# Optimization experiments

Measured on AMD Instinct MI355X. Metric: run time of the kernel, lower is better.

Reference implementation:

```python
import jax, jax.numpy as jnp
import numpy as np

B, S, H2 = 32, 4096, 512  # H2 = 2*hidden_size


def setup_inputs() -> dict:
    key = jax.random.key(0)
    ks = jax.random.split(key, 10)
    s = 1.0 / np.sqrt(H2)
    return {
        "decoder_state": jax.random.normal(ks[0], (B, 1, H2), jnp.float32),
        "encoder_outputs": jax.random.normal(ks[1], (B, S, H2), jnp.float32),
        "coverage_vector": jax.random.uniform(ks[2], (B, S, H2), jnp.float32),
        "W_h": jax.random.uniform(ks[3], (H2, H2), jnp.float32, -s, s),
        "b_h": jax.random.uniform(ks[4], (H2,), jnp.float32, -s, s),
        "W_s": jax.random.uniform(ks[5], (H2, H2), jnp.float32, -s, s),
        "b_s": jax.random.uniform(ks[6], (H2,), jnp.float32, -s, s),
        "W_c": jax.random.uniform(ks[7], (H2, H2), jnp.float32, -s, s),
        "b_c": jax.random.uniform(ks[8], (H2,), jnp.float32, -s, s),
        "v": jax.random.uniform(ks[9], (H2, 1), jnp.float32, -s, s),
    }


def reference(decoder_state, encoder_outputs, coverage_vector,
              W_h, b_h, W_s, b_s, W_c, b_c, v):
    # additive attention features: [B, S, 2H]
    e = jnp.tanh(encoder_outputs @ W_h + b_h
                 + decoder_state @ W_s + b_s      # broadcasts over S
                 + coverage_vector @ W_c + b_c)
    scores = e @ v                                # [B, S, 1]
    attn_dist = jax.nn.softmax(scores, axis=1)    # softmax over source positions
    # weighted sum of encoder outputs: [B, 1, 2H]
    h_star_t = jnp.einsum('bsi,bsd->bid', attn_dist, encoder_outputs)
    coverage_new = coverage_vector + attn_dist    # broadcast over feature dim
    return h_star_t, attn_dist, coverage_new
```

## Files before the change

### kernel.cpp

```cpp
#include <hip/hip_runtime.h>
#include <hip/hip_bf16.h>
#include <stdint.h>

#define H2    512
#define BATCH 32
#define SEQ   4096
#define BM    64
#define BK    64
#define NKT   16

typedef __attribute__((ext_vector_type(4))) float f32x4;
typedef __attribute__((ext_vector_type(8))) short bf16x8;

__device__ __forceinline__ unsigned short f2bf(float f) {
    union { float f; unsigned u; } v; v.f = f;
    unsigned r = v.u + 0x7FFF + ((v.u >> 16) & 1);
    return (unsigned short)(r >> 16);
}

__device__ __forceinline__ float fast_tanh(float x) {
    float e = __builtin_amdgcn_exp2f(x * 2.88539008177793f);
    return 1.0f - 2.0f * __builtin_amdgcn_rcpf(e + 1.0f);
}

__global__ void kprep_w(const float* __restrict__ Wh, const float* __restrict__ Wc,
                        unsigned short* __restrict__ wt) {
    int c    = blockIdx.x * blockDim.x + threadIdx.x;
    int lane = c & 63;
    int cb   = (c >> 6) & 31;
    int ks   = (c >> 11) & 1;
    int kt   = c >> 12;
    int col  = cb * 16 + (lane & 15);
    int k0   = kt * 64 + ks * 32 + (lane >> 4) * 8;
    unsigned short tmp[8];
#pragma unroll
    for (int j = 0; j < 8; ++j) {
        int kg = k0 + j;
        float w = (kg < 512) ? Wh[kg * 512 + col] : Wc[(kg - 512) * 512 + col];
        tmp[j] = f2bf(w);
    }
    *reinterpret_cast<uint4*>(wt + (size_t)c * 8) = *reinterpret_cast<const uint4*>(tmp);
}

__global__ void kprep_q(const float* __restrict__ dec, const float* __restrict__ Ws,
                        const float* __restrict__ bh, const float* __restrict__ bs,
                        const float* __restrict__ bc, float* __restrict__ q) {
    __shared__ float dsh[512];
    int b = blockIdx.x, t = threadIdx.x;
    dsh[t]       = dec[b * 512 + t];
    dsh[t + 256] = dec[b * 512 + 256 + t];
    __syncthreads();
    float a0 = 0.f, a1 = 0.f;
#pragma unroll 4
    for (int k = 0; k < 512; ++k) {
        float d = dsh[k];
        a0 = fmaf(d, Ws[k * 512 + t], a0);
        a1 = fmaf(d, Ws[k * 512 + 256 + t], a1);
    }
    q[b * 512 + t]       = a0 + bh[t] + bs[t] + bc[t];
    q[b * 512 + 256 + t] = a1 + bh[256 + t] + bs[256 + t] + bc[256 + t];
}

__launch_bounds__(512, 4)
__global__ void kgemm(const float* __restrict__ enc, const float* __restrict__ cov,
                      const unsigned short* __restrict__ wt,
                      const float* __restrict__ q, const float* __restrict__ vvec,
                      float* __restrict__ scores) {
    __shared__ unsigned short Asm[2][BM * BK];
    __shared__ float qv[H2];
    __shared__ float vv[H2];
    __shared__ float sred[BM][8];

    int tid  = threadIdx.x;
    int lane = tid & 63, wn = tid >> 6;

    int cpx  = gridDim.x >> 3;
    int swz  = (blockIdx.x & 7) * cpx + (blockIdx.x >> 3);
    int row0 = swz * BM;

    qv[tid] = q[(row0 >> 12) * H2 + tid];
    vv[tid] = vvec[tid];

    int r = tid >> 3, k8 = tid & 7;
    const float* ae = enc + (size_t)(row0 + r) * H2 + k8 * 8;
    const float* ac = cov + (size_t)(row0 + r) * H2 + k8 * 8;
    unsigned awb = (unsigned)(r * 128 + ((k8 * 16) ^ ((r & 7) << 4)));

    unsigned arb0 = (unsigned)((lane & 15) * 128 +
                    ((((lane >> 4) << 4))      ^ ((lane & 7) << 4)));
    unsigned arb1 = (unsigned)((lane & 15) * 128 +
                    (((64 + ((lane >> 4) << 4))) ^ ((lane & 7) << 4)));

    f32x4 acc[4][4] = {};

    {
        f32x4 a0 = *reinterpret_cast<const f32x4*>(ae);
        f32x4 a1 = *reinterpret_cast<const f32x4*>(ae + 4);
        union { unsigned short h[8]; uint4 u; } t;
#pragma unroll
        for (int j = 0; j < 4; ++j) { t.h[j] = f2bf(a0[j]); t.h[4 + j] = f2bf(a1[j]); }
        *reinterpret_cast<uint4*>((char*)Asm[0] + awb) = t.u;
    }
    __syncthreads();

    for (int kt = 0; kt < NKT; ++kt) {
        int cur = kt & 1;
        bf16x8 bfr[2][4];
        const bf16x8* bp0 = reinterpret_cast<const bf16x8*>(wt) +
                            ((size_t)(kt * 2 + 0) * 32 + wn * 4) * 64 + lane;
        const bf16x8* bp1 = reinterpret_cast<const bf16x8*>(wt) +
                            ((size_t)(kt * 2 + 1) * 32 + wn * 4) * 64 + lane;
#pragma unroll
        for (int ni = 0; ni < 4; ++ni) bfr[0][ni] = bp0[ni * 64];
#pragma unroll
        for (int ni = 0; ni < 4; ++ni) bfr[1][ni] = bp1[ni * 64];
        f32x4 p0, p1;
        if (kt + 1 < NKT) {
            const float* src = (kt + 1 < 8) ? (ae + (kt + 1) * 64) : (ac + (kt - 7) * 64);
            p0 = *reinterpret_cast<const f32x4*>(src);
            p1 = *reinterpret_cast<const f32x4*>(src + 4);
        }
#pragma unroll
        for (int ks = 0; ks < 2; ++ks) {
            bf16x8 af[4];
#pragma unroll
            for (int mi = 0; mi < 4; ++mi)
                af[mi] = *reinterpret_cast<const bf16x8*>(
                    (const char*)Asm[cur] + mi * 2048 + (ks ? arb1 : arb0));
#pragma unroll
            for (int mi = 0; mi < 4; ++mi)
#pragma unroll
                for (int ni = 0; ni < 4; ++ni)
                    acc[mi][ni] = __builtin_amdgcn_mfma_f32_16x16x32_bf16(
                        af[mi], bfr[ks][ni], acc[mi][ni], 0, 0, 0);
        }
        if (kt + 1 < NKT) {
            union { unsigned short h[8]; uint4 u; } t;
#pragma unroll
            for (int j = 0; j < 4; ++j) { t.h[j] = f2bf(p0[j]); t.h[4 + j] = f2bf(p1[j]); }
            *reinterpret_cast<uint4*>((char*)Asm[cur ^ 1] + awb) = t.u;
        }
        __syncthreads();
    }

    float ps[4][4] = {};
#pragma unroll
    for (int mi = 0; mi < 4; ++mi)
#pragma unroll
        for (int ni = 0; ni < 4; ++ni) {
            int colg = wn * 64 + ni * 16 + (lane & 15);
            float qq = qv[colg], vl = vv[colg];
#pragma unroll
            for (int j = 0; j < 4; ++j) {
                float e = fast_tanh(acc[mi][ni][j] + qq);
                ps[mi][j] = fmaf(e, vl, ps[mi][j]);
            }
        }
#pragma unroll
    for (int mi = 0; mi < 4; ++mi)
#pragma unroll
        for (int j = 0; j < 4; ++j) {
            float s = ps[mi][j];
            s += __shfl_xor(s, 1);
            s += __shfl_xor(s, 2);
            s += __shfl_xor(s, 4);
            s += __shfl_xor(s, 8);
            if ((lane & 15) == 0)
                sred[mi * 16 + (lane >> 4) * 4 + j][wn] = s;
        }
    __syncthreads();
    if (tid < BM) {
        float s = 0.f;
#pragma unroll
        for (int w = 0; w < 8; ++w) s += sred[tid][w];
        scores[row0 + tid] = s;
    }
}

__global__ void ksoftmax(const float* __restrict__ scores, float* __restrict__ out) {
    __shared__ float redm[16];
    __shared__ float reds[16];
    int b = blockIdx.x, t = threadIdx.x, lane = t & 63, w = t >> 6;
    if (t < 512) out[b * 512 + t] = 0.0f;
    f32x4 sv = *reinterpret_cast<const f32x4*>(scores + b * 4096 + t * 4);
    float m = fmaxf(fmaxf(sv[0], sv[1]), fmaxf(sv[2], sv[3]));
#pragma unroll
    for (int o = 1; o < 64; o <<= 1) m = fmaxf(m, __shfl_xor(m, o));
    if (lane == 0) redm[w] = m;
    __syncthreads();
    float mm = redm[0];
#pragma unroll
    for (int i = 1; i < 16; ++i) mm = fmaxf(mm, redm[i]);

    f32x4 p;
#pragma unroll
    for (int j = 0; j < 4; ++j)
        p[j] = __builtin_amdgcn_exp2f((sv[j] - mm) * 1.4426950408889634f);
    float s = p[0] + p[1] + p[2] + p[3];
#pragma unroll
    for (int o = 1; o < 64; o <<= 1) s += __shfl_xor(s, o);
    if (lane == 0) reds[w] = s;
    __syncthreads();
    float tot = 0.f;
#pragma unroll
    for (int i = 0; i < 16; ++i) tot += reds[i];
    float rinv = __builtin_amdgcn_rcpf(tot);
    p *= rinv;
    *reinterpret_cast<f32x4*>(out + 16384 + b * 4096 + t * 4) = p;
}

__global__ void kcov(const float* __restrict__ enc, const float* __restrict__ cov,
                     float* __restrict__ out) {
    const float* attn = out + 16384;
    float* covn  = out + 16384 + 131072;
    float* hstar = out;
    int blk = blockIdx.x;
    int b = blk >> 6, ck = blk & 63;
    int s0 = ck * 64;
    int t  = threadIdx.x;
    int f4 = (t & 127) * 4;
    int rp = t >> 7;
    size_t base = (size_t)b * SEQ * H2;
    f32x4 h = {0.f, 0.f, 0.f, 0.f};
#pragma unroll 2
    for (int i = 0; i < 32; ++i) {
        int s = s0 + i * 2 + rp;
        float a = attn[b * 4096 + s];
        size_t idx = base + (size_t)s * H2 + f4;
        f32x4 e4 = *reinterpret_cast<const f32x4*>(enc + idx);
        f32x4 c4 = *reinterpret_cast<const f32x4*>(cov + idx);
        c4 += a;
        __builtin_nontemporal_store(c4, reinterpret_cast<f32x4*>(covn + idx));
        h += a * e4;
    }
    int off = b * 512 + f4;
    atomicAdd(&hstar[off + 0], h[0]);
    atomicAdd(&hstar[off + 1], h[1]);
    atomicAdd(&hstar[off + 2], h[2]);
    atomicAdd(&hstar[off + 3], h[3]);
}

extern "C" void kernel_launch(void* const* d_in, const int* in_sizes, int n_in,
                              void* d_out, int out_size, void* d_ws, size_t ws_size,
                              hipStream_t stream) {
    const float* dec = (const float*)d_in[0];
    const float* enc = (const float*)d_in[1];
    const float* cov = (const float*)d_in[2];
    const float* Wh  = (const float*)d_in[3];
    const float* bh  = (const float*)d_in[4];
    const float* Ws  = (const float*)d_in[5];
    const float* bs  = (const float*)d_in[6];
    const float* Wc  = (const float*)d_in[7];
    const float* bc  = (const float*)d_in[8];
    const float* v   = (const float*)d_in[9];
    float* out = (float*)d_out;

    char* ws = (char*)d_ws;
    unsigned short* wt = (unsigned short*)ws;
    float* q      = (float*)(ws + (1 << 20));
    float* scores = (float*)(ws + (1 << 20) + 65536);

    kprep_w <<<dim3(256),  dim3(256),  0, stream>>>(Wh, Wc, wt);
    kprep_q <<<dim3(32),   dim3(256),  0, stream>>>(dec, Ws, bh, bs, bc, q);
    kgemm   <<<dim3(2048), dim3(512),  0, stream>>>(enc, cov, wt, q, v, scores);
    ksoftmax<<<dim3(32),   dim3(1024), 0, stream>>>(scores, out);
    kcov    <<<dim3(2048), dim3(256),  0, stream>>>(enc, cov, out);
}
```

Baseline: 401.5 us.

## Load A fragments directly from global into registers, dropping LDS staging and barriers

The GEMM kernel no longer stages encoder/coverage tiles through shared memory with per-step barriers. Each wave now loads its A fragments straight from global memory, converts them with packed bf16 conversion instructions, and splits waves 2x4 over rows and columns with a 32x128 per-wave tile. The weight prep layout changes to 32-wide k-steps, and s_setprio is placed around the MFMA blocks. This removes LDS traffic and synchronisation. In exchange, A rows are loaded redundantly by the 4 column waves, and global loads are less coalesced with only a small prefetch distance.

```diff
diff --git a/kernel.cpp b/kernel.cpp
--- a/kernel.cpp
+++ b/kernel.cpp
@@ -6,8 +6,6 @@
 #define BATCH 32
 #define SEQ   4096
 #define BM    64
-#define BK    64
-#define NKT   16
 
 typedef __attribute__((ext_vector_type(4))) float f32x4;
 typedef __attribute__((ext_vector_type(8))) short bf16x8;
@@ -16,6 +14,15 @@
     union { float f; unsigned u; } v; v.f = f;
     unsigned r = v.u + 0x7FFF + ((v.u >> 16) & 1);
     return (unsigned short)(r >> 16);
+}
+
+__device__ __forceinline__ bf16x8 cvt8_bf16(f32x4 lo, f32x4 hi) {
+    union { uint4 u; bf16x8 h; } r;
+    asm("v_cvt_pk_bf16_f32 %0, %1, %2" : "=v"(r.u.x) : "v"(lo[0]), "v"(lo[1]));
+    asm("v_cvt_pk_bf16_f32 %0, %1, %2" : "=v"(r.u.y) : "v"(lo[2]), "v"(lo[3]));
+    asm("v_cvt_pk_bf16_f32 %0, %1, %2" : "=v"(r.u.z) : "v"(hi[0]), "v"(hi[1]));
+    asm("v_cvt_pk_bf16_f32 %0, %1, %2" : "=v"(r.u.w) : "v"(hi[2]), "v"(hi[3]));
+    return r.h;
 }
 
 __device__ __forceinline__ float fast_tanh(float x) {
@@ -28,10 +35,9 @@
     int c    = blockIdx.x * blockDim.x + threadIdx.x;
     int lane = c & 63;
     int cb   = (c >> 6) & 31;
-    int ks   = (c >> 11) & 1;
-    int kt   = c >> 12;
+    int kt   = c >> 11;
     int col  = cb * 16 + (lane & 15);
-    int k0   = kt * 64 + ks * 32 + (lane >> 4) * 8;
+    int k0   = kt * 32 + (lane >> 4) * 8;
     unsigned short tmp[8];
 #pragma unroll
     for (int j = 0; j < 8; ++j) {
@@ -66,13 +72,13 @@
                       const unsigned short* __restrict__ wt,
                       const float* __restrict__ q, const float* __restrict__ vvec,
                       float* __restrict__ scores) {
-    __shared__ unsigned short Asm[2][BM * BK];
     __shared__ float qv[H2];
     __shared__ float vv[H2];
-    __shared__ float sred[BM][8];
+    __shared__ float sred[BM][4];
 
     int tid  = threadIdx.x;
-    int lane = tid & 63, wn = tid >> 6;
+    int lane = tid & 63, wid = tid >> 6;
+    int wm   = wid >> 2, wn = wid & 3;
 
     int cpx  = gridDim.x >> 3;
     int swz  = (blockIdx.x & 7) * cpx + (blockIdx.x >> 3);
@@ -81,74 +87,62 @@
     qv[tid] = q[(row0 >> 12) * H2 + tid];
     vv[tid] = vvec[tid];
 
-    int r = tid >> 3, k8 = tid & 7;
-    const float* ae = enc + (size_t)(row0 + r) * H2 + k8 * 8;
-    const float* ac = cov + (size_t)(row0 + r) * H2 + k8 * 8;
-    unsigned awb = (unsigned)(r * 128 + ((k8 * 16) ^ ((r & 7) << 4)));
-
-    unsigned arb0 = (unsigned)((lane & 15) * 128 +
-                    ((((lane >> 4) << 4))      ^ ((lane & 7) << 4)));
-    unsigned arb1 = (unsigned)((lane & 15) * 128 +
-                    (((64 + ((lane >> 4) << 4))) ^ ((lane & 7) << 4)));
-
-    f32x4 acc[4][4] = {};
-
-    {
-        f32x4 a0 = *reinterpret_cast<const f32x4*>(ae);
-        f32x4 a1 = *reinterpret_cast<const f32x4*>(ae + 4);
-        union { unsigned short h[8]; uint4 u; } t;
-#pragma unroll
-        for (int j = 0; j < 4; ++j) { t.h[j] = f2bf(a0[j]); t.h[4 + j] = f2bf(a1[j]); }
-        *reinterpret_cast<uint4*>((char*)Asm[0] + awb) = t.u;
-    }
-    __syncthreads();
-
-    for (int kt = 0; kt < NKT; ++kt) {
-        int cur = kt & 1;
-        bf16x8 bfr[2][4];
-        const bf16x8* bp0 = reinterpret_cast<const bf16x8*>(wt) +
-                            ((size_t)(kt * 2 + 0) * 32 + wn * 4) * 64 + lane;
-        const bf16x8* bp1 = reinterpret_cast<const bf16x8*>(wt) +
-                            ((size_t)(kt * 2 + 1) * 32 + wn * 4) * 64 + lane;
-#pragma unroll
-        for (int ni = 0; ni < 4; ++ni) bfr[0][ni] = bp0[ni * 64];
-#pragma unroll
-        for (int ni = 0; ni < 4; ++ni) bfr[1][ni] = bp1[ni * 64];
-        f32x4 p0, p1;
-        if (kt + 1 < NKT) {
-            const float* src = (kt + 1 < 8) ? (ae + (kt + 1) * 64) : (ac + (kt - 7) * 64);
-            p0 = *reinterpret_cast<const f32x4*>(src);
-            p1 = *reinterpret_cast<const f32x4*>(src + 4);
-        }
-#pragma unroll
-        for (int ks = 0; ks < 2; ++ks) {
-            bf16x8 af[4];
-#pragma unroll
-            for (int mi = 0; mi < 4; ++mi)
-                af[mi] = *reinterpret_cast<const bf16x8*>(
-                    (const char*)Asm[cur] + mi * 2048 + (ks ? arb1 : arb0));
-#pragma unroll
-            for (int mi = 0; mi < 4; ++mi)
+    const float* ap = enc + (size_t)(row0 + wm * 32 + (lane & 15)) * H2 +
+                      ((lane >> 4) << 3);
+    const float* cp = cov + (size_t)(row0 + wm * 32 + (lane & 15)) * H2 +
+                      ((lane >> 4) << 3);
+    const bf16x8* bb = reinterpret_cast<const bf16x8*>(wt) +
+                       (size_t)(wn * 8) * 64 + lane;
+
+    f32x4 acc[2][8] = {};
+
+    const float* asrc = ap;
+#pragma unroll 1
+    for (int half = 0; half < 2; ++half) {
+#pragma unroll 2
+        for (int t = 0; t < 16; ++t) {
+            const int kt = half * 16 + t;
+            bf16x8 bf[4];
+#pragma unroll
+            for (int ni = 0; ni < 4; ++ni)
+                bf[ni] = bb[(size_t)kt * 2048 + ni * 64];
+            bf16x8 af[2];
+#pragma unroll
+            for (int mi = 0; mi < 2; ++mi) {
+                f32x4 lo = *reinterpret_cast<const f32x4*>(asrc + mi * 8192 + t * 32);
+                f32x4 hi = *reinterpret_cast<const f32x4*>(asrc + mi * 8192 + t * 32 + 4);
+                af[mi] = cvt8_bf16(lo, hi);
+            }
+            __builtin_amdgcn_s_setprio(1);
+#pragma unroll
+            for (int mi = 0; mi < 2; ++mi)
 #pragma unroll
                 for (int ni = 0; ni < 4; ++ni)
                     acc[mi][ni] = __builtin_amdgcn_mfma_f32_16x16x32_bf16(
-                        af[mi], bfr[ks][ni], acc[mi][ni], 0, 0, 0);
+                        af[mi], bf[ni], acc[mi][ni], 0, 0, 0);
+            __builtin_amdgcn_s_setprio(0);
+#pragma unroll
+            for (int ni = 0; ni < 4; ++ni)
+                bf[ni] = bb[(size_t)kt * 2048 + (ni + 4) * 64];
+            __builtin_amdgcn_s_setprio(1);
+#pragma unroll
+            for (int mi = 0; mi < 2; ++mi)
+#pragma unroll
+                for (int ni = 0; ni < 4; ++ni)
+                    acc[mi][ni + 4] = __builtin_amdgcn_mfma_f32_16x16x32_bf16(
+                        af[mi], bf[ni], acc[mi][ni + 4], 0, 0, 0);
+            __builtin_amdgcn_s_setprio(0);
         }
-        if (kt + 1 < NKT) {
-            union { unsigned short h[8]; uint4 u; } t;
-#pragma unroll
-            for (int j = 0; j < 4; ++j) { t.h[j] = f2bf(p0[j]); t.h[4 + j] = f2bf(p1[j]); }
-            *reinterpret_cast<uint4*>((char*)Asm[cur ^ 1] + awb) = t.u;
-        }
-        __syncthreads();
-    }
-
-    float ps[4][4] = {};
-#pragma unroll
-    for (int mi = 0; mi < 4; ++mi)
-#pragma unroll
-        for (int ni = 0; ni < 4; ++ni) {
-            int colg = wn * 64 + ni * 16 + (lane & 15);
+        asrc = cp;
+    }
+
+    __syncthreads();
+    float ps[2][4] = {};
+#pragma unroll
+    for (int mi = 0; mi < 2; ++mi)
+#pragma unroll
+        for (int ni = 0; ni < 8; ++ni) {
+            int colg = wn * 128 + ni * 16 + (lane & 15);
             float qq = qv[colg], vl = vv[colg];
 #pragma unroll
             for (int j = 0; j < 4; ++j) {
@@ -157,7 +151,7 @@
             }
         }
 #pragma unroll
-    for (int mi = 0; mi < 4; ++mi)
+    for (int mi = 0; mi < 2; ++mi)
 #pragma unroll
         for (int j = 0; j < 4; ++j) {
             float s = ps[mi][j];
@@ -166,13 +160,11 @@
             s += __shfl_xor(s, 4);
             s += __shfl_xor(s, 8);
             if ((lane & 15) == 0)
-                sred[mi * 16 + (lane >> 4) * 4 + j][wn] = s;
+                sred[wm * 32 + mi * 16 + (lane >> 4) * 4 + j][wn] = s;
         }
     __syncthreads();
     if (tid < BM) {
-        float s = 0.f;
-#pragma unroll
-        for (int w = 0; w < 8; ++w) s += sred[tid][w];
+        float s = sred[tid][0] + sred[tid][1] + sred[tid][2] + sred[tid][3];
         scores[row0 + tid] = s;
     }
 }
```

After: 617.1 us. 53.7% more time.
